# Performance work log

Hardware: AMD Instinct MI355X
Metric: run time of the kernel (lower is better)

The kernel has to match this reference:

```python
import jax, jax.numpy as jnp
import numpy as np

CODEBOOK_SIZE = 1024
EMBED_DIM = 64
COMMITMENT_COST = 0.25


def setup_inputs() -> dict:
    key = jax.random.key(0)
    k1, k2 = jax.random.split(key)
    z = jax.random.normal(k1, (8, EMBED_DIM, 8192), dtype=jnp.float32)
    # torch init: uniform(-1/codebook_size, 1/codebook_size)
    codebook_weight = jax.random.uniform(
        k2, (CODEBOOK_SIZE, EMBED_DIM), dtype=jnp.float32,
        minval=-1.0 / CODEBOOK_SIZE, maxval=1.0 / CODEBOOK_SIZE)
    return {"z": z, "codebook_weight": codebook_weight}


def reference(z, codebook_weight):
    B, D, T = z.shape
    # [B*T, D]
    z_flat = jnp.transpose(z, (0, 2, 1)).reshape(-1, D)
    # squared euclidean distances to each code: ||z||^2 - 2 z.W^T + ||W||^2
    distances = (jnp.sum(z_flat * z_flat, axis=1, keepdims=True)
                 - 2.0 * z_flat @ codebook_weight.T
                 + jnp.sum(codebook_weight * codebook_weight, axis=1))
    codes = jnp.argmin(distances, axis=1)  # [B*T]
    z_q = codebook_weight[codes].reshape(B, T, D).transpose(0, 2, 1)  # [B, D, T]
    commitment_loss = jnp.mean((jax.lax.stop_gradient(z_q) - z) ** 2)
    codebook_loss = jnp.mean((z_q - jax.lax.stop_gradient(z)) ** 2)
    vq_loss = codebook_loss + COMMITMENT_COST * commitment_loss
    # straight-through estimator
    z_q_st = z + jax.lax.stop_gradient(z_q - z)
    return z_q_st, vq_loss, codes
```

## Files before the change

### kernel.cpp

```cpp
#include <hip/hip_runtime.h>


#define T_DIM 8192
#define D_DIM 64
#define C_DIM 1024
#define B_DIM 8
#define NROWS (B_DIM * T_DIM)
#define NELEM (B_DIM * D_DIM * T_DIM)
#define SEGS 4
#define CODES_PER_SEG (C_DIM / SEGS)
#define EPI_BLOCKS (NELEM / 4 / 256)

#define R64(M) M(0) M(1) M(2) M(3) M(4) M(5) M(6) M(7) \
  M(8) M(9) M(10) M(11) M(12) M(13) M(14) M(15) \
  M(16) M(17) M(18) M(19) M(20) M(21) M(22) M(23) \
  M(24) M(25) M(26) M(27) M(28) M(29) M(30) M(31) \
  M(32) M(33) M(34) M(35) M(36) M(37) M(38) M(39) \
  M(40) M(41) M(42) M(43) M(44) M(45) M(46) M(47) \
  M(48) M(49) M(50) M(51) M(52) M(53) M(54) M(55) \
  M(56) M(57) M(58) M(59) M(60) M(61) M(62) M(63)

#define SQ_(x) __fmul_rn(x, x)
#define AD_(a, b) __fadd_rn(a, b)

#define PAIRWISE64(p, dst) \
  float pr0 = SQ_(p##0);  pr0 = AD_(pr0, SQ_(p##8));  pr0 = AD_(pr0, SQ_(p##16)); pr0 = AD_(pr0, SQ_(p##24)); pr0 = AD_(pr0, SQ_(p##32)); pr0 = AD_(pr0, SQ_(p##40)); pr0 = AD_(pr0, SQ_(p##48)); pr0 = AD_(pr0, SQ_(p##56)); \
  float pr1 = SQ_(p##1);  pr1 = AD_(pr1, SQ_(p##9));  pr1 = AD_(pr1, SQ_(p##17)); pr1 = AD_(pr1, SQ_(p##25)); pr1 = AD_(pr1, SQ_(p##33)); pr1 = AD_(pr1, SQ_(p##41)); pr1 = AD_(pr1, SQ_(p##49)); pr1 = AD_(pr1, SQ_(p##57)); \
  float pr2 = SQ_(p##2);  pr2 = AD_(pr2, SQ_(p##10)); pr2 = AD_(pr2, SQ_(p##18)); pr2 = AD_(pr2, SQ_(p##26)); pr2 = AD_(pr2, SQ_(p##34)); pr2 = AD_(pr2, SQ_(p##42)); pr2 = AD_(pr2, SQ_(p##50)); pr2 = AD_(pr2, SQ_(p##58)); \
  float pr3 = SQ_(p##3);  pr3 = AD_(pr3, SQ_(p##11)); pr3 = AD_(pr3, SQ_(p##19)); pr3 = AD_(pr3, SQ_(p##27)); pr3 = AD_(pr3, SQ_(p##35)); pr3 = AD_(pr3, SQ_(p##43)); pr3 = AD_(pr3, SQ_(p##51)); pr3 = AD_(pr3, SQ_(p##59)); \
  float pr4 = SQ_(p##4);  pr4 = AD_(pr4, SQ_(p##12)); pr4 = AD_(pr4, SQ_(p##20)); pr4 = AD_(pr4, SQ_(p##28)); pr4 = AD_(pr4, SQ_(p##36)); pr4 = AD_(pr4, SQ_(p##44)); pr4 = AD_(pr4, SQ_(p##52)); pr4 = AD_(pr4, SQ_(p##60)); \
  float pr5 = SQ_(p##5);  pr5 = AD_(pr5, SQ_(p##13)); pr5 = AD_(pr5, SQ_(p##21)); pr5 = AD_(pr5, SQ_(p##29)); pr5 = AD_(pr5, SQ_(p##37)); pr5 = AD_(pr5, SQ_(p##45)); pr5 = AD_(pr5, SQ_(p##53)); pr5 = AD_(pr5, SQ_(p##61)); \
  float pr6 = SQ_(p##6);  pr6 = AD_(pr6, SQ_(p##14)); pr6 = AD_(pr6, SQ_(p##22)); pr6 = AD_(pr6, SQ_(p##30)); pr6 = AD_(pr6, SQ_(p##38)); pr6 = AD_(pr6, SQ_(p##46)); pr6 = AD_(pr6, SQ_(p##54)); pr6 = AD_(pr6, SQ_(p##62)); \
  float pr7 = SQ_(p##7);  pr7 = AD_(pr7, SQ_(p##15)); pr7 = AD_(pr7, SQ_(p##23)); pr7 = AD_(pr7, SQ_(p##31)); pr7 = AD_(pr7, SQ_(p##39)); pr7 = AD_(pr7, SQ_(p##47)); pr7 = AD_(pr7, SQ_(p##55)); pr7 = AD_(pr7, SQ_(p##63)); \
  float dst = AD_(AD_(AD_(pr0, pr1), AD_(pr2, pr3)), AD_(AD_(pr4, pr5), AD_(pr6, pr7)));

__global__ __launch_bounds__(256, 4)
void vq_dist_kernel(const float* __restrict__ z,
                    const float* __restrict__ cb,
                    float2* __restrict__ pairs) {
    const int row = blockIdx.x * 256 + threadIdx.x;
    const int seg = blockIdx.y;
    const int c0 = seg * CODES_PER_SEG;
    const int b = row >> 13;
    const int t = row & (T_DIM - 1);

    __shared__ float wsqs[CODES_PER_SEG];
    {
        const float* wp = cb + ((size_t)(c0 + threadIdx.x) << 6);
#define LOADW(k) float w##k = wp[k];
        R64(LOADW)
#undef LOADW
        PAIRWISE64(w, s)
        wsqs[threadIdx.x] = s;
    }
    __syncthreads();

    const float* zp = z + (size_t)b * (D_DIM * T_DIM) + t;
#define LOADZ(k) float z##k = zp[(size_t)k * T_DIM]; \
                 asm volatile("" : "+v"(z##k));
    R64(LOADZ)
#undef LOADZ

    PAIRWISE64(z, zsq)

    float bestd = 3.4e38f;
    int besti = 0;
#pragma unroll 1
    for (int cc = 0; cc < CODES_PER_SEG; cc += 4) {
        const float* wpa = cb + ((size_t)(c0 + cc) << 6);
        const float* wpb = wpa + 64;
        const float* wpc = wpa + 128;
        const float* wpd = wpa + 192;
        float a0 = 0.f, a1 = 0.f, a2 = 0.f, a3 = 0.f;
#define DOT4(k) a0 = fmaf(z##k, wpa[k], a0); \
                a1 = fmaf(z##k, wpb[k], a1); \
                a2 = fmaf(z##k, wpc[k], a2); \
                a3 = fmaf(z##k, wpd[k], a3);
        R64(DOT4)
#undef DOT4
        float d0 = __fadd_rn(__fsub_rn(zsq, __fmul_rn(2.0f, a0)), wsqs[cc + 0]);
        float d1 = __fadd_rn(__fsub_rn(zsq, __fmul_rn(2.0f, a1)), wsqs[cc + 1]);
        float d2 = __fadd_rn(__fsub_rn(zsq, __fmul_rn(2.0f, a2)), wsqs[cc + 2]);
        float d3 = __fadd_rn(__fsub_rn(zsq, __fmul_rn(2.0f, a3)), wsqs[cc + 3]);
        if (d0 < bestd) { bestd = d0; besti = c0 + cc + 0; }
        if (d1 < bestd) { bestd = d1; besti = c0 + cc + 1; }
        if (d2 < bestd) { bestd = d2; besti = c0 + cc + 2; }
        if (d3 < bestd) { bestd = d3; besti = c0 + cc + 3; }
    }
    pairs[seg * NROWS + row] = make_float2(bestd, (float)besti);
}

__global__ void vq_argmin_kernel(const float2* __restrict__ pairs,
                                 float* __restrict__ codes) {
    int row = blockIdx.x * blockDim.x + threadIdx.x;
    float2 best = pairs[row];
#pragma unroll
    for (int s = 1; s < SEGS; ++s) {
        float2 p = pairs[s * NROWS + row];
        if (p.x < best.x) best = p;
    }
    codes[row] = best.y;
}

__global__ void vq_epilogue_kernel(const float* __restrict__ z,
                                   const float* __restrict__ cb,
                                   const float* __restrict__ codes,
                                   float* __restrict__ out,
                                   double* __restrict__ partials) {
    const int q = blockIdx.x * 256 + threadIdx.x;
    const int i = q << 2;
    const int t = i & (T_DIM - 1);
    const int bd = i >> 13;
    const int d = bd & (D_DIM - 1);
    const int b = bd >> 6;
    const int row = (b << 13) | t;

    float4 cr = *(const float4*)(codes + row);
    float4 zv = *(const float4*)(z + i);
    float w0 = cb[((int)cr.x << 6) + d];
    float w1 = cb[((int)cr.y << 6) + d];
    float w2 = cb[((int)cr.z << 6) + d];
    float w3 = cb[((int)cr.w << 6) + d];

    float4 df = make_float4(w0 - zv.x, w1 - zv.y, w2 - zv.z, w3 - zv.w);
    float4 o = make_float4(zv.x + df.x, zv.y + df.y, zv.z + df.z, zv.w + df.w);
    *(float4*)(out + i) = o;

    double v = (double)df.x * df.x + (double)df.y * df.y +
               (double)df.z * df.z + (double)df.w * df.w;
#pragma unroll
    for (int o2 = 32; o2 > 0; o2 >>= 1) v += __shfl_down(v, o2, 64);

    __shared__ double red[4];
    if ((threadIdx.x & 63) == 0) red[threadIdx.x >> 6] = v;
    __syncthreads();
    if (threadIdx.x == 0)
        partials[blockIdx.x] = ((red[0] + red[1]) + (red[2] + red[3]));
}

__global__ void vq_loss_kernel(const double* __restrict__ partials,
                               float* __restrict__ out_loss) {
    double s = 0.0;
    for (int i = threadIdx.x; i < EPI_BLOCKS; i += 256) s += partials[i];
#pragma unroll
    for (int o = 32; o > 0; o >>= 1) s += __shfl_down(s, o, 64);
    __shared__ double red[4];
    if ((threadIdx.x & 63) == 0) red[threadIdx.x >> 6] = s;
    __syncthreads();
    if (threadIdx.x == 0) {
        double tot = (red[0] + red[1]) + (red[2] + red[3]);
        out_loss[0] = (float)(1.25 * tot / (double)NELEM);
    }
}

extern "C" void kernel_launch(void* const* d_in, const int* in_sizes, int n_in,
                              void* d_out, int out_size, void* d_ws, size_t ws_size,
                              hipStream_t stream) {
    const float* z  = (const float*)d_in[0];
    const float* cb = (const float*)d_in[1];

    float* out      = (float*)d_out;
    float* out_loss = out + NELEM;
    float* codes    = out + NELEM + 1;

    char* ws    = (char*)d_ws;
    double* partials = (double*)(ws);
    float2* pairs = (float2*)(ws + 32768);

    dim3 grid1(NROWS / 256, SEGS);
    vq_dist_kernel<<<grid1, 256, 0, stream>>>(z, cb, pairs);

    vq_argmin_kernel<<<NROWS / 256, 256, 0, stream>>>(pairs, codes);

    vq_epilogue_kernel<<<EPI_BLOCKS, 256, 0, stream>>>(z, cb, codes, out, partials);

    vq_loss_kernel<<<1, 256, 0, stream>>>(partials, out_loss);
}
```

Measured before the change: 264.0 us.

## Stage z rows in LDS and compute eight codes per iteration

The distance kernel now stores each thread's 64-element z vector in shared memory as float4s, instead of keeping all 64 values pinned in registers. It processes eight codebook entries per loop iteration instead of four. The intent is to free registers and reuse each z load across more codes, cutting the number of loop iterations and the scalar codebook loads per FMA. The cost is 64KB of LDS per block and a lower occupancy hint (2 blocks per CU instead of 4). Every z value is now re-read from LDS once per iteration, which may become the bottleneck.

```diff
diff --git a/kernel.cpp b/kernel.cpp
--- a/kernel.cpp
+++ b/kernel.cpp
@@ -34,58 +34,90 @@
   float pr7 = SQ_(p##7);  pr7 = AD_(pr7, SQ_(p##15)); pr7 = AD_(pr7, SQ_(p##23)); pr7 = AD_(pr7, SQ_(p##31)); pr7 = AD_(pr7, SQ_(p##39)); pr7 = AD_(pr7, SQ_(p##47)); pr7 = AD_(pr7, SQ_(p##55)); pr7 = AD_(pr7, SQ_(p##63)); \
   float dst = AD_(AD_(AD_(pr0, pr1), AD_(pr2, pr3)), AD_(AD_(pr4, pr5), AD_(pr6, pr7)));
 
-__global__ __launch_bounds__(256, 4)
+__global__ __launch_bounds__(256, 2)
 void vq_dist_kernel(const float* __restrict__ z,
                     const float* __restrict__ cb,
                     float2* __restrict__ pairs) {
-    const int row = blockIdx.x * 256 + threadIdx.x;
+    const int tid = threadIdx.x;
+    const int row = blockIdx.x * 256 + tid;
     const int seg = blockIdx.y;
     const int c0 = seg * CODES_PER_SEG;
     const int b = row >> 13;
     const int t = row & (T_DIM - 1);
 
     __shared__ float wsqs[CODES_PER_SEG];
+    __shared__ float4 zl[16][256];
+
     {
-        const float* wp = cb + ((size_t)(c0 + threadIdx.x) << 6);
+        const float* wp = cb + ((size_t)(c0 + tid) << 6);
 #define LOADW(k) float w##k = wp[k];
         R64(LOADW)
 #undef LOADW
         PAIRWISE64(w, s)
-        wsqs[threadIdx.x] = s;
-    }
-    __syncthreads();
+        wsqs[tid] = s;
+    }
 
     const float* zp = z + (size_t)b * (D_DIM * T_DIM) + t;
-#define LOADZ(k) float z##k = zp[(size_t)k * T_DIM]; \
-                 asm volatile("" : "+v"(z##k));
+#define LOADZ(k) float z##k = zp[(size_t)k * T_DIM];
     R64(LOADZ)
 #undef LOADZ
-
     PAIRWISE64(z, zsq)
+    zl[ 0][tid] = make_float4(z0,  z1,  z2,  z3);
+    zl[ 1][tid] = make_float4(z4,  z5,  z6,  z7);
+    zl[ 2][tid] = make_float4(z8,  z9,  z10, z11);
+    zl[ 3][tid] = make_float4(z12, z13, z14, z15);
+    zl[ 4][tid] = make_float4(z16, z17, z18, z19);
+    zl[ 5][tid] = make_float4(z20, z21, z22, z23);
+    zl[ 6][tid] = make_float4(z24, z25, z26, z27);
+    zl[ 7][tid] = make_float4(z28, z29, z30, z31);
+    zl[ 8][tid] = make_float4(z32, z33, z34, z35);
+    zl[ 9][tid] = make_float4(z36, z37, z38, z39);
+    zl[10][tid] = make_float4(z40, z41, z42, z43);
+    zl[11][tid] = make_float4(z44, z45, z46, z47);
+    zl[12][tid] = make_float4(z48, z49, z50, z51);
+    zl[13][tid] = make_float4(z52, z53, z54, z55);
+    zl[14][tid] = make_float4(z56, z57, z58, z59);
+    zl[15][tid] = make_float4(z60, z61, z62, z63);
+    __syncthreads();
 
     float bestd = 3.4e38f;
     int besti = 0;
 #pragma unroll 1
-    for (int cc = 0; cc < CODES_PER_SEG; cc += 4) {
-        const float* wpa = cb + ((size_t)(c0 + cc) << 6);
-        const float* wpb = wpa + 64;
-        const float* wpc = wpa + 128;
-        const float* wpd = wpa + 192;
+    for (int cc = 0; cc < CODES_PER_SEG; cc += 8) {
+        const float* wp = cb + ((size_t)(c0 + cc) << 6);
         float a0 = 0.f, a1 = 0.f, a2 = 0.f, a3 = 0.f;
-#define DOT4(k) a0 = fmaf(z##k, wpa[k], a0); \
-                a1 = fmaf(z##k, wpb[k], a1); \
-                a2 = fmaf(z##k, wpc[k], a2); \
-                a3 = fmaf(z##k, wpd[k], a3);
-        R64(DOT4)
-#undef DOT4
-        float d0 = __fadd_rn(__fsub_rn(zsq, __fmul_rn(2.0f, a0)), wsqs[cc + 0]);
-        float d1 = __fadd_rn(__fsub_rn(zsq, __fmul_rn(2.0f, a1)), wsqs[cc + 1]);
-        float d2 = __fadd_rn(__fsub_rn(zsq, __fmul_rn(2.0f, a2)), wsqs[cc + 2]);
-        float d3 = __fadd_rn(__fsub_rn(zsq, __fmul_rn(2.0f, a3)), wsqs[cc + 3]);
+        float a4 = 0.f, a5 = 0.f, a6 = 0.f, a7 = 0.f;
+#pragma unroll
+        for (int kk = 0; kk < 16; ++kk) {
+            const float4 zk = zl[kk][tid];
+            const int k4 = kk << 2;
+#define CHAIN(n) \
+            a##n = fmaf(zk.x, wp[(n << 6) + k4 + 0], a##n); \
+            a##n = fmaf(zk.y, wp[(n << 6) + k4 + 1], a##n); \
+            a##n = fmaf(zk.z, wp[(n << 6) + k4 + 2], a##n); \
+            a##n = fmaf(zk.w, wp[(n << 6) + k4 + 3], a##n);
+            CHAIN(0) CHAIN(1) CHAIN(2) CHAIN(3)
+            CHAIN(4) CHAIN(5) CHAIN(6) CHAIN(7)
+#undef CHAIN
+        }
+        const float4 wqA = *(const float4*)(&wsqs[cc]);
+        const float4 wqB = *(const float4*)(&wsqs[cc + 4]);
+        float d0 = __fadd_rn(__fsub_rn(zsq, __fmul_rn(2.0f, a0)), wqA.x);
+        float d1 = __fadd_rn(__fsub_rn(zsq, __fmul_rn(2.0f, a1)), wqA.y);
+        float d2 = __fadd_rn(__fsub_rn(zsq, __fmul_rn(2.0f, a2)), wqA.z);
+        float d3 = __fadd_rn(__fsub_rn(zsq, __fmul_rn(2.0f, a3)), wqA.w);
+        float d4 = __fadd_rn(__fsub_rn(zsq, __fmul_rn(2.0f, a4)), wqB.x);
+        float d5 = __fadd_rn(__fsub_rn(zsq, __fmul_rn(2.0f, a5)), wqB.y);
+        float d6 = __fadd_rn(__fsub_rn(zsq, __fmul_rn(2.0f, a6)), wqB.z);
+        float d7 = __fadd_rn(__fsub_rn(zsq, __fmul_rn(2.0f, a7)), wqB.w);
         if (d0 < bestd) { bestd = d0; besti = c0 + cc + 0; }
         if (d1 < bestd) { bestd = d1; besti = c0 + cc + 1; }
         if (d2 < bestd) { bestd = d2; besti = c0 + cc + 2; }
         if (d3 < bestd) { bestd = d3; besti = c0 + cc + 3; }
+        if (d4 < bestd) { bestd = d4; besti = c0 + cc + 4; }
+        if (d5 < bestd) { bestd = d5; besti = c0 + cc + 5; }
+        if (d6 < bestd) { bestd = d6; besti = c0 + cc + 6; }
+        if (d7 < bestd) { bestd = d7; besti = c0 + cc + 7; }
     }
     pairs[seg * NROWS + row] = make_float2(bestd, (float)besti);
 }
```

Result: no change. 268.2 us (+1.6%).
